# Performance work log

Hardware: AMD Instinct MI355X
Metric: run time of the kernel (lower is better)

## Reference

```python
import jax, jax.numpy as jnp
import numpy as np
from jax import lax

B, T, H, V, P, L = 256, 100, 1024, 47, 3, 3
BEGIN_IDX = 1  # SmilesCharDictionary.begin_idx


def setup_inputs() -> dict:
    key = jax.random.key(0)
    ks = jax.random.split(key, 10)
    s = 0.05
    return {
        "x": jax.random.randint(ks[0], (B, T), 0, V),
        "properties": jax.random.normal(ks[1], (B, P), dtype=jnp.float32),
        "h0": jnp.zeros((L, B, H), jnp.float32),
        "c0": jnp.zeros((L, B, H), jnp.float32),
        "E": jax.random.normal(ks[2], (V, H), dtype=jnp.float32) * s,
        "W_ih0": jax.random.normal(ks[3], (4 * H, H + P), dtype=jnp.float32) * s,
        "W_hh0": jax.random.normal(ks[4], (4 * H, H), dtype=jnp.float32) * s,
        "b_ih0": jnp.zeros((4 * H,), jnp.float32),
        "b_hh0": jnp.zeros((4 * H,), jnp.float32),
        "W_ih_r": jax.random.normal(ks[5], (L - 1, 4 * H, H), dtype=jnp.float32) * s,
        "W_hh_r": jax.random.normal(ks[6], (L - 1, 4 * H, H), dtype=jnp.float32) * s,
        "b_ih_r": jnp.zeros((L - 1, 4 * H), jnp.float32),
        "b_hh_r": jnp.zeros((L - 1, 4 * H), jnp.float32),
        "W_dec": jax.random.normal(ks[7], (V, H), dtype=jnp.float32) * s,
        "b_dec": jnp.zeros((V,), jnp.float32),
        "seq_len": T,
    }


def _lstm_cell(gates, c):
    # PyTorch gate order: i, f, g, o
    i, f, g, o = jnp.split(gates, 4, axis=-1)
    i = jax.nn.sigmoid(i)
    f = jax.nn.sigmoid(f)
    o = jax.nn.sigmoid(o)
    g = jnp.tanh(g)
    c_new = f * c + i * g
    return o * jnp.tanh(c_new), c_new


def _forward(x, properties, h0, c0, E, W_ih0, W_hh0, b_ih0, b_hh0,
             W_ih_r, W_hh_r, b_ih_r, b_hh_r, W_dec, b_dec, seq_len):
    b = properties.shape[0]
    steps = seq_len - 1  # loop runs t = 1 .. seq_len-1
    # Teacher-forcing inputs: [begin, x[:,1], ..., x[:,seq_len-2]] (x[:,0] is unused)
    begin = jnp.full((b, 1), BEGIN_IDX, dtype=x.dtype)
    tokens = jnp.concatenate([begin, x[:, 1:seq_len - 1]], axis=1)  # [B, steps]
    emb = E[tokens]  # [B, steps, H]
    props = jnp.broadcast_to(properties[:, None, :], (b, steps, properties.shape[1]))
    inp0 = jnp.concatenate([emb, props], axis=-1)  # [B, steps, H+P]
    # Precompute layer-0 input contribution to the gates (one big GEMM)
    gx0 = jnp.einsum('bti,gi->btg', inp0, W_ih0) + b_ih0  # [B, steps, 4H]

    n_layers = h0.shape[0]

    def step(carry, gx_t):
        h, c = carry  # each [L, B, H]
        gates = gx_t + h[0] @ W_hh0.T + b_hh0
        h_new, c_new = _lstm_cell(gates, c[0])
        hs, cs = [h_new], [c_new]
        xl = h_new
        for l in range(n_layers - 1):
            gates = xl @ W_ih_r[l].T + b_ih_r[l] + h[l + 1] @ W_hh_r[l].T + b_hh_r[l]
            h_new, c_new = _lstm_cell(gates, c[l + 1])
            hs.append(h_new)
            cs.append(c_new)
            xl = h_new
        return (jnp.stack(hs), jnp.stack(cs)), xl

    (hT, cT), outs = lax.scan(step, (h0, c0), gx0.transpose(1, 0, 2))
    outs = outs.transpose(1, 0, 2)  # [B, steps, H]
    logits = jnp.einsum('bth,vh->btv', outs, W_dec) + b_dec  # [B, steps, V]
    return logits, hT, cT


def reference(x, properties, h0, c0, E, W_ih0, W_hh0, b_ih0, b_hh0,
              W_ih_r, W_hh_r, b_ih_r, b_hh_r, W_dec, b_dec, seq_len):
    return _forward(x, properties, h0, c0, E, W_ih0, W_hh0, b_ih0, b_hh0,
                    W_ih_r, W_hh_r, b_ih_r, b_hh_r, W_dec, b_dec, seq_len)
```

## Files before the change

kernel.cpp:

```cpp
#include <hip/hip_runtime.h>


typedef unsigned short u16;
typedef __bf16 bf16x8 __attribute__((ext_vector_type(8)));
typedef float f32x4 __attribute__((ext_vector_type(4)));
typedef u16 u16x8 __attribute__((ext_vector_type(8)));

#define MFMA16(a,b,c) __builtin_amdgcn_mfma_f32_16x16x32_bf16((a),(b),(c),0,0,0)
#define BH 262144

__device__ __forceinline__ u16 f2bf(float f){
  unsigned u = __builtin_bit_cast(unsigned, f);
  u += 0x7fffu + ((u >> 16) & 1u);
  return (u16)(u >> 16);
}
__device__ __forceinline__ float bf2f(u16 s){
  unsigned u = ((unsigned)s) << 16;
  return __builtin_bit_cast(float, u);
}
__device__ __forceinline__ float sigm(float x){ return 1.f/(1.f+__expf(-x)); }
__device__ __forceinline__ float tanhfast(float x){ return 1.f - 2.f/(__expf(2.f*x)+1.f); }

__device__ __forceinline__ void ld_lds16(const u16* g, u16* l){
  __builtin_amdgcn_global_load_lds((const __attribute__((address_space(1))) void*)g,
                                   (__attribute__((address_space(3))) void*)l, 16, 0, 0);
}

__global__ void k_conv(const float* __restrict__ src, u16* __restrict__ dst,
                       long total, int srow, int sstride, int dstride, int doff){
  long i = ((long)blockIdx.x*blockDim.x + threadIdx.x)*8;
  if (i >= total) return;
  long r = i / srow;
  int  k = (int)(i - r*srow);
  const float* s = src + r*(long)sstride + k;
  u16x8 o;
  #pragma unroll
  for (int j=0;j<8;++j) o[j] = f2bf(s[j]);
  *(u16x8*)(dst + r*(long)dstride + doff + k) = o;
}

__global__ void k_repackB(const float* __restrict__ Wih, const float* __restrict__ Whh,
                          u16* __restrict__ dst, int nkt){
  long p = (long)blockIdx.x*256 + threadIdx.x;
  int G = (int)(p & 511);
  long q = p >> 9;
  int kt = (int)(q % nkt);
  int jt = (int)(q / nkt);
  int r = G >> 3, s = G & 7;
  int kk = kt*64 + ((s ^ (r & 7)) << 3);
  int n = (r >> 4)*1024 + jt*16 + (r & 15);
  const float* src = (kk < 1024) ? Wih + (size_t)n*1024 + kk
                                 : Whh + (size_t)n*1024 + (kk - 1024);
  u16x8 o;
  #pragma unroll
  for (int j=0;j<8;++j) o[j] = f2bf(src[j]);
  *(u16x8*)(dst + p*8) = o;
}

__global__ void k_misc(const float* __restrict__ b_ih0, const float* __restrict__ b_hh0,
                       const float* __restrict__ b_ihr, const float* __restrict__ b_hhr,
                       const float* __restrict__ h0, const float* __restrict__ c0,
                       const float* __restrict__ props, const float* __restrict__ W_ih0,
                       u16* __restrict__ Ebf, u16* __restrict__ Wdec,
                       float* __restrict__ bias0, float* __restrict__ bcat,
                       u16* __restrict__ hist0, u16* __restrict__ hist1,
                       u16* __restrict__ outsbF,
                       float* __restrict__ cst, float* __restrict__ gxp){
  long i = (long)blockIdx.x*256 + threadIdx.x;
  if (i < 4096){ bias0[i] = b_ih0[i] + b_hh0[i]; return; }
  i -= 4096;
  if (i < 2*4096){ bcat[i] = b_ihr[i] + b_hhr[i]; return; }
  i -= 2*4096;
  if (i < 1024){ Ebf[47*1024 + i] = 0; Wdec[47*1024 + i] = 0; return; }
  i -= 1024;
  if (i < (long)3*BH){
    int l = (int)(i >> 18); long r = i & (BH-1);
    u16 v = f2bf(h0[i]);
    if (l==0)      hist0[(size_t)7*BH + r] = v;
    else if (l==1) hist1[(size_t)7*BH + r] = v;
    else           outsbF[r] = v;
    cst[i] = c0[i];
    return;
  }
  i -= (long)3*BH;
  if (i < (long)256*4096){
    int b = (int)(i >> 12), n = (int)(i & 4095);
    const float* wr = W_ih0 + (long)n*1027 + 1024;
    gxp[i] = props[b*3+0]*wr[0] + props[b*3+1]*wr[1] + props[b*3+2]*wr[2];
  }
}

__global__ __launch_bounds__(64)
void k_gxemb(const u16* __restrict__ Ebf, const u16* __restrict__ Wih0b, float* __restrict__ gxe){
  const int lane = threadIdx.x;
  const int cl = lane & 15, ko = (lane >> 4)*8;
  const int m0 = blockIdx.x*16;
  const int n0 = blockIdx.y*16;
  f32x4 acc = {0.f,0.f,0.f,0.f};
  const u16* ap = Ebf   + (size_t)(m0+cl)*1024 + ko;
  const u16* bp = Wih0b + (size_t)(n0+cl)*1024 + ko;
  for (int k0=0; k0<1024; k0+=32){
    bf16x8 a = *(const bf16x8*)(ap + k0);
    bf16x8 b = *(const bf16x8*)(bp + k0);
    acc = MFMA16(a, b, acc);
  }
  const int rbase = (lane >> 4)*4;
  #pragma unroll
  for (int q=0;q<4;++q){
    int v = m0 + rbase + q;
    if (v < 47) gxe[(size_t)v*4096 + n0 + cl] = acc[q];
  }
}

#define KLOOP_BODY(APTR_EXPR)                                                   \
  auto stage = [&](int s, int kt){                                              \
    const int kbase = kt*64;                                                    \
    u16* sA = lds + (size_t)s*12288;                                            \
    u16* sB = sA + 8192;                                                        \
    _Pragma("unroll")                                                           \
    for (int j=0;j<4;++j){                                                      \
      int G = j*256 + tid; int r = G >> 3;                                      \
      int kk = kbase + (((G & 7) ^ (r & 7)) << 3);                              \
      ld_lds16(APTR_EXPR, sA + (size_t)G*8);                                    \
    }                                                                           \
    _Pragma("unroll")                                                           \
    for (int j=0;j<2;++j){                                                      \
      int G = j*256 + tid;                                                      \
      ld_lds16(Bblk + (size_t)kt*4096 + (size_t)G*8, sB + (size_t)G*8);         \
    }                                                                           \
  };                                                                            \
  f32x4 acc[2][4];                                                              \
  _Pragma("unroll")                                                             \
  for (int mf=0; mf<2; ++mf)                                                    \
    _Pragma("unroll")                                                           \
    for (int g=0; g<4; ++g) acc[mf][g] = (f32x4){0.f,0.f,0.f,0.f};              \
  stage(0,0); stage(1,1);                                                       \
  for (int kt=0; kt<16; ++kt){                                                  \
    if (kt == 15) asm volatile("s_waitcnt vmcnt(0)" ::: "memory");              \
    else          asm volatile("s_waitcnt vmcnt(6)" ::: "memory");              \
    __builtin_amdgcn_s_barrier();                                               \
    asm volatile("" ::: "memory");                                              \
    if (kt+2 < 16) stage((kt+2)%3, kt+2);                                       \
    const u16* A = lds + (size_t)(kt%3)*12288;                                  \
    const u16* B = A + 8192;                                                    \
    __builtin_amdgcn_s_setprio(1);                                              \
    _Pragma("unroll")                                                           \
    for (int half=0; half<2; ++half){                                           \
      const int kg = half*4 + hi;                                               \
      bf16x8 a0, a1, b[4];                                                      \
      { int r = m0w + cl;      a0 = *(const bf16x8*)(A + r*64 + ((kg ^ (r&7))<<3)); } \
      { int r = m0w + 16 + cl; a1 = *(const bf16x8*)(A + r*64 + ((kg ^ (r&7))<<3)); } \
      _Pragma("unroll")                                                         \
      for (int g=0; g<4; ++g){                                                  \
        int r = g*16 + cl;                                                      \
        b[g] = *(const bf16x8*)(B + r*64 + ((kg ^ (r&7))<<3));                  \
      }                                                                         \
      _Pragma("unroll")                                                         \
      for (int g=0; g<4; ++g){                                                  \
        acc[0][g] = MFMA16(a0, b[g], acc[0][g]);                                \
        acc[1][g] = MFMA16(a1, b[g], acc[1][g]);                                \
      }                                                                         \
    }                                                                           \
    __builtin_amdgcn_s_setprio(0);                                              \
    asm volatile("" ::: "memory");                                              \
  }

template<int LAYER>
__device__ __forceinline__ void diagh_tile(int mt, int jt, int t,
    const int* __restrict__ x, const u16* hp, u16* aux, float* cc,
    const u16* __restrict__ Bblk, const float* __restrict__ bias,
    const float* __restrict__ gxe, const float* __restrict__ gxp,
    const u16* xpt, u16* lds)
{
  const int tid = threadIdx.x;
  const int lane = tid & 63, w = tid >> 6;
  const int cl = lane & 15, hi = lane >> 4;
  const int m_base = mt*128, m0w = w*32;

  KLOOP_BODY(hp + (size_t)(m_base + r)*1024 + kk)

  const int hcol = jt*16 + cl;
  const float bi_ = bias[hcol], bf_ = bias[1024+hcol],
              bg_ = bias[2048+hcol], bo_ = bias[3072+hcol];
  #pragma unroll
  for (int mf=0; mf<2; ++mf){
    #pragma unroll
    for (int q=0; q<4; ++q){
      const int row = m_base + m0w + mf*16 + hi*4 + q;
      float gi = acc[mf][0][q] + bi_;
      float gf = acc[mf][1][q] + bf_;
      float gg = acc[mf][2][q] + bg_;
      float go = acc[mf][3][q] + bo_;
      if (LAYER == 0){
        const int tok = (t==0) ? 1 : x[row*100 + t];
        const float* ge = gxe + (size_t)tok*4096;
        const float* gp = gxp + (size_t)row*4096;
        gi += ge[hcol]        + gp[hcol];
        gf += ge[1024 + hcol] + gp[1024 + hcol];
        gg += ge[2048 + hcol] + gp[2048 + hcol];
        go += ge[3072 + hcol] + gp[3072 + hcol];
      } else {
        const u16* xr = xpt + (size_t)row*4096;
        gi += bf2f(xr[hcol]);
        gf += bf2f(xr[1024 + hcol]);
        gg += bf2f(xr[2048 + hcol]);
        go += bf2f(xr[3072 + hcol]);
      }
      const float i_ = sigm(gi), f_ = sigm(gf), o_ = sigm(go), g_ = tanhfast(gg);
      const size_t off = (size_t)row*1024 + hcol;
      const float cn = f_*cc[off] + i_*g_;
      cc[off] = cn;
      aux[off] = f2bf(o_*tanhfast(cn));
    }
  }
}

__device__ __forceinline__ void xp_tile(int m_base, int jt,
    const u16* hp, const u16* __restrict__ Bblk, u16* xpo, u16* lds)
{
  const int tid = threadIdx.x;
  const int lane = tid & 63, w = tid >> 6;
  const int cl = lane & 15, hi = lane >> 4;
  const int m0w = w*32;

  KLOOP_BODY(hp + (size_t)(m_base + r)*1024 + kk)

  const int hcol = jt*16 + cl;
  #pragma unroll
  for (int mf=0; mf<2; ++mf){
    #pragma unroll
    for (int q=0; q<4; ++q){
      const int m = m_base + m0w + mf*16 + hi*4 + q;
      u16* xr = xpo + (size_t)m*4096 + hcol;
      xr[0]    = f2bf(acc[mf][0][q]);
      xr[1024] = f2bf(acc[mf][1][q]);
      xr[2048] = f2bf(acc[mf][2][q]);
      xr[3072] = f2bf(acc[mf][3][q]);
    }
  }
}

__global__ __launch_bounds__(256)
void k_diag(int d, const int* __restrict__ x, u16* hist0, u16* hist1, u16* outsbF,
            float* __restrict__ cst, const u16* __restrict__ WpkH,
            const u16* __restrict__ WpkI,
            const float* __restrict__ bias0, const float* __restrict__ bcat,
            const float* __restrict__ gxe, const float* __restrict__ gxp,
            u16* __restrict__ xpb1, u16* __restrict__ xpb2)
{
  extern __shared__ u16 lds[];
  const int id = blockIdx.x;
  if (id < 384){
    const int mt = id / 192;
    const int slot = id - mt*192;
    const int layer = slot >> 6;
    const int jt = slot & 63;
    const int t = d - 3*layer;
    if (t < 0 || t > 98) return;
    if (layer == 0){
      diagh_tile<0>(mt, jt, t, x, hist0 + (size_t)((t+7)&7)*BH, hist0 + (size_t)(t&7)*BH,
                    cst, WpkH + (size_t)jt*65536, bias0, gxe, gxp, nullptr, lds);
    } else if (layer == 1){
      const u16* xpt = xpb1 + (size_t)((((t>>1)&1)<<1) + (t&1))*1048576;
      diagh_tile<1>(mt, jt, t, x, hist1 + (size_t)((t+7)&7)*BH, hist1 + (size_t)(t&7)*BH,
                    cst + BH, WpkH + (size_t)4194304 + (size_t)jt*65536, bcat,
                    nullptr, nullptr, xpt, lds);
    } else {
      const u16* xpt = xpb2 + (size_t)((((t>>1)&1)<<1) + (t&1))*1048576;
      diagh_tile<2>(mt, jt, t, x, outsbF + (size_t)t*BH, outsbF + (size_t)(t+1)*BH,
                    cst + 2*BH, WpkH + (size_t)8388608 + (size_t)jt*65536, bcat + 4096,
                    nullptr, nullptr, xpt, lds);
    }
  } else {
    const int idx = id - 384;
    const int mtx = idx >> 6, jt = idx & 63;
    const int tsub = mtx >> 1, m_base = (mtx & 1)*128;
    int w; const u16* hist; const u16* Wblk; u16* xpo;
    if ((d & 1) == 0){ w = (d-2)>>1; hist = hist0; Wblk = WpkI;                     xpo = xpb1; }
    else             { w = (d-5)>>1; hist = hist1; Wblk = WpkI + (size_t)4194304;   xpo = xpb2; }
    const int t = 2*w + tsub;
    if (t > 98) return;
    xp_tile(m_base, jt, hist + (size_t)(t&7)*BH, Wblk + (size_t)jt*65536,
            xpo + (size_t)(((w&1)<<1) + tsub)*1048576, lds);
  }
}

__global__ __launch_bounds__(256)
void k_decode(const u16* __restrict__ outs, const u16* __restrict__ Wdec,
              const float* __restrict__ bdec, float* __restrict__ logits){
  const int lane = threadIdx.x & 63, w = threadIdx.x >> 6;
  const int cl = lane & 15, ko = (lane >> 4)*8;
  const size_t m0 = ((size_t)blockIdx.x*4 + w)*16;
  const u16* ap = outs + (m0+cl)*1024 + ko;
  f32x4 acc[3];
  #pragma unroll
  for (int nt=0; nt<3; ++nt) acc[nt] = (f32x4){0.f,0.f,0.f,0.f};
  const u16* bp = Wdec + (size_t)cl*1024 + ko;
  for (int k0=0; k0<1024; k0+=32){
    bf16x8 a = *(const bf16x8*)(ap + k0);
    #pragma unroll
    for (int nt=0; nt<3; ++nt){
      bf16x8 b = *(const bf16x8*)(bp + (size_t)nt*16*1024 + k0);
      acc[nt] = MFMA16(a, b, acc[nt]);
    }
  }
  const int rbase = (lane >> 4)*4;
  #pragma unroll
  for (int nt=0; nt<3; ++nt){
    #pragma unroll
    for (int q=0; q<4; ++q){
      int v = nt*16 + cl;
      if (v < 47){
        size_t row = m0 + rbase + q;
        int tt = (int)(row >> 8);
        int b  = (int)(row & 255);
        logits[((size_t)b*99 + tt)*47 + v] = acc[nt][q] + bdec[v];
      }
    }
  }
}

__global__ void k_final(const u16* __restrict__ h0s, const u16* __restrict__ h1s,
                        const u16* __restrict__ h2s, const float* __restrict__ cst,
                        float* __restrict__ out){
  long i = (long)blockIdx.x*256 + threadIdx.x;
  if (i < (long)3*BH){
    int l = (int)(i >> 18); long r = i & (BH-1);
    const u16* src = (l==0) ? h0s : (l==1) ? h1s : h2s;
    out[1191168 + i] = bf2f(src[r]);
    out[1191168 + 786432 + i] = cst[i];
  }
}

extern "C" void kernel_launch(void* const* d_in, const int* in_sizes, int n_in,
                              void* d_out, int out_size, void* d_ws, size_t ws_size,
                              hipStream_t stream) {
  (void)in_sizes; (void)n_in; (void)out_size; (void)ws_size;
  const int*   x      = (const int*)  d_in[0];
  const float* props  = (const float*)d_in[1];
  const float* h0     = (const float*)d_in[2];
  const float* c0     = (const float*)d_in[3];
  const float* E      = (const float*)d_in[4];
  const float* W_ih0  = (const float*)d_in[5];
  const float* W_hh0  = (const float*)d_in[6];
  const float* b_ih0  = (const float*)d_in[7];
  const float* b_hh0  = (const float*)d_in[8];
  const float* W_ih_r = (const float*)d_in[9];
  const float* W_hh_r = (const float*)d_in[10];
  const float* b_ih_r = (const float*)d_in[11];
  const float* b_hh_r = (const float*)d_in[12];
  const float* W_dec  = (const float*)d_in[13];
  const float* b_dec  = (const float*)d_in[14];
  float* out = (float*)d_out;

  u16* WpkH   = (u16*)d_ws;
  u16* WpkI   = WpkH  + (size_t)12582912;
  u16* Wdec   = WpkI  + (size_t)8388608;
  u16* Ebf    = Wdec  + (size_t)49152;
  u16* hist0  = Ebf   + (size_t)49152;
  u16* hist1  = hist0 + (size_t)8*BH;
  u16* outsbF = hist1 + (size_t)8*BH;
  u16* xpb1   = outsbF + (size_t)100*BH;
  u16* xpb2   = xpb1  + (size_t)4194304;
  u16* Wih0b  = xpb1;
  float* gxe   = (float*)(xpb2 + (size_t)4194304);
  float* gxp   = gxe   + (size_t)196608;
  float* bias0 = gxp   + (size_t)1048576;
  float* bcat  = bias0 + 4096;
  float* cst   = bcat  + 8192;

  k_repackB<<<2048, 256, 0, stream>>>(W_hh0, W_hh0, WpkH, 16);
  k_repackB<<<2048, 256, 0, stream>>>(W_hh_r, W_hh_r, WpkH + (size_t)4194304, 16);
  k_repackB<<<2048, 256, 0, stream>>>(W_hh_r + (size_t)4194304, W_hh_r + (size_t)4194304,
                                      WpkH + (size_t)8388608, 16);
  k_repackB<<<2048, 256, 0, stream>>>(W_ih_r, W_ih_r, WpkI, 16);
  k_repackB<<<2048, 256, 0, stream>>>(W_ih_r + (size_t)4194304, W_ih_r + (size_t)4194304,
                                      WpkI + (size_t)4194304, 16);
  k_conv<<<2048, 256, 0, stream>>>(W_ih0, Wih0b, (long)4096*1024, 1024, 1027, 1024, 0);
  k_conv<<<24,   256, 0, stream>>>(E,     Ebf,   (long)47*1024,   1024, 1024, 1024, 0);
  k_conv<<<24,   256, 0, stream>>>(W_dec, Wdec,  (long)47*1024,   1024, 1024, 1024, 0);
  k_misc<<<7221, 256, 0, stream>>>(b_ih0, b_hh0, b_ih_r, b_hh_r, h0, c0, props, W_ih0,
                                   Ebf, Wdec, bias0, bcat, hist0, hist1, outsbF, cst, gxp);
  k_gxemb<<<dim3(3,256), 64, 0, stream>>>(Ebf, Wih0b, gxe);

  (void)hipFuncSetAttribute(reinterpret_cast<const void*>(k_diag),
                            hipFuncAttributeMaxDynamicSharedMemorySize, 73728);
  for (int d = 0; d <= 104; ++d){
    bool hx = ((d & 1) == 0) ? (d >= 2 && d <= 100) : (d >= 5 && d <= 103);
    k_diag<<<384 + (hx ? 256 : 0), 256, 73728, stream>>>(
        d, x, hist0, hist1, outsbF, cst, WpkH, WpkI,
        bias0, bcat, gxe, gxp, xpb1, xpb2);
  }

  k_decode<<<396, 256, 0, stream>>>(outsbF + (size_t)BH, Wdec, b_dec, out);
  k_final<<<3072, 256, 0, stream>>>(hist0 + (size_t)2*BH, hist1 + (size_t)2*BH,
                                    outsbF + (size_t)99*BH, cst, out);
}
```

Before: 2.475 ms.

## Batch input projections over four timesteps and prefetch weights to L2

Restructures the diagonal wavefront schedule so the inter-layer input projections are computed for four timesteps per batch instead of two. Layers are now skewed by five diagonals and the xp buffers are doubled to hold four slots. Extra global_load_lds prefetches of weight tiles into a throwaway LDS region warm the cache ahead of use, with vmcnt waits adjusted to match. The layer-0 input-gate tables are stored as bf16 to cut bandwidth. The trade-offs are more launches (109 vs 105), larger LDS and workspace use, and some precision loss in the layer-0 gate contributions.

```diff
diff --git a/kernel.cpp b/kernel.cpp
--- a/kernel.cpp
+++ b/kernel.cpp
@@ -65,7 +65,7 @@
                        float* __restrict__ bias0, float* __restrict__ bcat,
                        u16* __restrict__ hist0, u16* __restrict__ hist1,
                        u16* __restrict__ outsbF,
-                       float* __restrict__ cst, float* __restrict__ gxp){
+                       float* __restrict__ cst, u16* __restrict__ gxp){
   long i = (long)blockIdx.x*256 + threadIdx.x;
   if (i < 4096){ bias0[i] = b_ih0[i] + b_hh0[i]; return; }
   i -= 4096;
@@ -86,12 +86,12 @@
   if (i < (long)256*4096){
     int b = (int)(i >> 12), n = (int)(i & 4095);
     const float* wr = W_ih0 + (long)n*1027 + 1024;
-    gxp[i] = props[b*3+0]*wr[0] + props[b*3+1]*wr[1] + props[b*3+2]*wr[2];
+    gxp[i] = f2bf(props[b*3+0]*wr[0] + props[b*3+1]*wr[1] + props[b*3+2]*wr[2]);
   }
 }
 
 __global__ __launch_bounds__(64)
-void k_gxemb(const u16* __restrict__ Ebf, const u16* __restrict__ Wih0b, float* __restrict__ gxe){
+void k_gxemb(const u16* __restrict__ Ebf, const u16* __restrict__ Wih0b, u16* __restrict__ gxe){
   const int lane = threadIdx.x;
   const int cl = lane & 15, ko = (lane >> 4)*8;
   const int m0 = blockIdx.x*16;
@@ -108,11 +108,12 @@
   #pragma unroll
   for (int q=0;q<4;++q){
     int v = m0 + rbase + q;
-    if (v < 47) gxe[(size_t)v*4096 + n0 + cl] = acc[q];
+    if (v < 47) gxe[(size_t)v*4096 + n0 + cl] = f2bf(acc[q]);
   }
 }
 
 #define KLOOP_BODY(APTR_EXPR)                                                   \
+  u16* const trash = lds + 36864;                                               \
   auto stage = [&](int s, int kt){                                              \
     const int kbase = kt*64;                                                    \
     u16* sA = lds + (size_t)s*12288;                                            \
@@ -129,6 +130,13 @@
       ld_lds16(Bblk + (size_t)kt*4096 + (size_t)G*8, sB + (size_t)G*8);         \
     }                                                                           \
   };                                                                            \
+  auto pret = [&](int kt){                                                      \
+    _Pragma("unroll")                                                           \
+    for (int j=0;j<2;++j){                                                      \
+      int G = j*256 + tid;                                                      \
+      ld_lds16(Bblk + (size_t)kt*4096 + (size_t)G*8, trash);                    \
+    }                                                                           \
+  };                                                                            \
   f32x4 acc[2][4];                                                              \
   _Pragma("unroll")                                                             \
   for (int mf=0; mf<2; ++mf)                                                    \
@@ -136,11 +144,16 @@
     for (int g=0; g<4; ++g) acc[mf][g] = (f32x4){0.f,0.f,0.f,0.f};              \
   stage(0,0); stage(1,1);                                                       \
   for (int kt=0; kt<16; ++kt){                                                  \
-    if (kt == 15) asm volatile("s_waitcnt vmcnt(0)" ::: "memory");              \
-    else          asm volatile("s_waitcnt vmcnt(6)" ::: "memory");              \
+    if (kt == 0)       asm volatile("s_waitcnt vmcnt(6)"  ::: "memory");        \
+    else if (kt == 1)  asm volatile("s_waitcnt vmcnt(8)"  ::: "memory");        \
+    else if (kt <= 12) asm volatile("s_waitcnt vmcnt(10)" ::: "memory");        \
+    else if (kt == 13) asm volatile("s_waitcnt vmcnt(8)"  ::: "memory");        \
+    else if (kt == 14) asm volatile("s_waitcnt vmcnt(6)"  ::: "memory");        \
+    else               asm volatile("s_waitcnt vmcnt(0)"  ::: "memory");        \
     __builtin_amdgcn_s_barrier();                                               \
     asm volatile("" ::: "memory");                                              \
     if (kt+2 < 16) stage((kt+2)%3, kt+2);                                       \
+    if (kt+4 < 16) pret(kt+4);                                                  \
     const u16* A = lds + (size_t)(kt%3)*12288;                                  \
     const u16* B = A + 8192;                                                    \
     __builtin_amdgcn_s_setprio(1);                                              \
@@ -169,7 +182,7 @@
 __device__ __forceinline__ void diagh_tile(int mt, int jt, int t,
     const int* __restrict__ x, const u16* hp, u16* aux, float* cc,
     const u16* __restrict__ Bblk, const float* __restrict__ bias,
-    const float* __restrict__ gxe, const float* __restrict__ gxp,
+    const u16* __restrict__ gxe, const u16* __restrict__ gxp,
     const u16* xpt, u16* lds)
 {
   const int tid = threadIdx.x;
@@ -193,12 +206,12 @@
       float go = acc[mf][3][q] + bo_;
       if (LAYER == 0){
         const int tok = (t==0) ? 1 : x[row*100 + t];
-        const float* ge = gxe + (size_t)tok*4096;
-        const float* gp = gxp + (size_t)row*4096;
-        gi += ge[hcol]        + gp[hcol];
-        gf += ge[1024 + hcol] + gp[1024 + hcol];
-        gg += ge[2048 + hcol] + gp[2048 + hcol];
-        go += ge[3072 + hcol] + gp[3072 + hcol];
+        const u16* ge = gxe + (size_t)tok*4096;
+        const u16* gp = gxp + (size_t)row*4096;
+        gi += bf2f(ge[hcol])        + bf2f(gp[hcol]);
+        gf += bf2f(ge[1024 + hcol]) + bf2f(gp[1024 + hcol]);
+        gg += bf2f(ge[2048 + hcol]) + bf2f(gp[2048 + hcol]);
+        go += bf2f(ge[3072 + hcol]) + bf2f(gp[3072 + hcol]);
       } else {
         const u16* xr = xpt + (size_t)row*4096;
         gi += bf2f(xr[hcol]);
@@ -245,7 +258,7 @@
             float* __restrict__ cst, const u16* __restrict__ WpkH,
             const u16* __restrict__ WpkI,
             const float* __restrict__ bias0, const float* __restrict__ bcat,
-            const float* __restrict__ gxe, const float* __restrict__ gxp,
+            const u16* __restrict__ gxe, const u16* __restrict__ gxp,
             u16* __restrict__ xpb1, u16* __restrict__ xpb2)
 {
   extern __shared__ u16 lds[];
@@ -255,33 +268,35 @@
     const int slot = id - mt*192;
     const int layer = slot >> 6;
     const int jt = slot & 63;
-    const int t = d - 3*layer;
+    const int t = d - 5*layer;
     if (t < 0 || t > 98) return;
     if (layer == 0){
       diagh_tile<0>(mt, jt, t, x, hist0 + (size_t)((t+7)&7)*BH, hist0 + (size_t)(t&7)*BH,
                     cst, WpkH + (size_t)jt*65536, bias0, gxe, gxp, nullptr, lds);
     } else if (layer == 1){
-      const u16* xpt = xpb1 + (size_t)((((t>>1)&1)<<1) + (t&1))*1048576;
+      const u16* xpt = xpb1 + (size_t)((((t>>2)&1)<<2) + (t&3))*1048576;
       diagh_tile<1>(mt, jt, t, x, hist1 + (size_t)((t+7)&7)*BH, hist1 + (size_t)(t&7)*BH,
                     cst + BH, WpkH + (size_t)4194304 + (size_t)jt*65536, bcat,
                     nullptr, nullptr, xpt, lds);
     } else {
-      const u16* xpt = xpb2 + (size_t)((((t>>1)&1)<<1) + (t&1))*1048576;
+      const u16* xpt = xpb2 + (size_t)((((t>>2)&1)<<2) + (t&3))*1048576;
       diagh_tile<2>(mt, jt, t, x, outsbF + (size_t)t*BH, outsbF + (size_t)(t+1)*BH,
                     cst + 2*BH, WpkH + (size_t)8388608 + (size_t)jt*65536, bcat + 4096,
                     nullptr, nullptr, xpt, lds);
     }
   } else {
     const int idx = id - 384;
-    const int mtx = idx >> 6, jt = idx & 63;
-    const int tsub = mtx >> 1, m_base = (mtx & 1)*128;
+    const int jt = idx & 63;
+    const int mtx = (idx >> 6) & 1;
+    const int tsub = idx >> 7;
+    const int m_base = mtx*128;
     int w; const u16* hist; const u16* Wblk; u16* xpo;
-    if ((d & 1) == 0){ w = (d-2)>>1; hist = hist0; Wblk = WpkI;                     xpo = xpb1; }
-    else             { w = (d-5)>>1; hist = hist1; Wblk = WpkI + (size_t)4194304;   xpo = xpb2; }
-    const int t = 2*w + tsub;
+    if ((d & 3) == 0){ w = (d-4)>>2; hist = hist0; Wblk = WpkI;                   xpo = xpb1; }
+    else             { w = (d-9)>>2; hist = hist1; Wblk = WpkI + (size_t)4194304; xpo = xpb2; }
+    const int t = 4*w + tsub;
     if (t > 98) return;
     xp_tile(m_base, jt, hist + (size_t)(t&7)*BH, Wblk + (size_t)jt*65536,
-            xpo + (size_t)(((w&1)<<1) + tsub)*1048576, lds);
+            xpo + (size_t)(((w&1)<<2) + tsub)*1048576, lds);
   }
 }
 
@@ -361,11 +376,11 @@
   u16* hist1  = hist0 + (size_t)8*BH;
   u16* outsbF = hist1 + (size_t)8*BH;
   u16* xpb1   = outsbF + (size_t)100*BH;
-  u16* xpb2   = xpb1  + (size_t)4194304;
+  u16* xpb2   = xpb1  + (size_t)8388608;
   u16* Wih0b  = xpb1;
-  float* gxe   = (float*)(xpb2 + (size_t)4194304);
-  float* gxp   = gxe   + (size_t)196608;
-  float* bias0 = gxp   + (size_t)1048576;
+  u16* gxe    = xpb2  + (size_t)8388608;
+  u16* gxp    = gxe   + (size_t)196608;
+  float* bias0 = (float*)(gxp + (size_t)1048576);
   float* bcat  = bias0 + 4096;
   float* cst   = bcat  + 8192;
 
@@ -384,10 +399,11 @@
   k_gxemb<<<dim3(3,256), 64, 0, stream>>>(Ebf, Wih0b, gxe);
 
   (void)hipFuncSetAttribute(reinterpret_cast<const void*>(k_diag),
-                            hipFuncAttributeMaxDynamicSharedMemorySize, 73728);
-  for (int d = 0; d <= 104; ++d){
-    bool hx = ((d & 1) == 0) ? (d >= 2 && d <= 100) : (d >= 5 && d <= 103);
-    k_diag<<<384 + (hx ? 256 : 0), 256, 73728, stream>>>(
+                            hipFuncAttributeMaxDynamicSharedMemorySize, 75776);
+  for (int d = 0; d <= 108; ++d){
+    bool hx = ((d & 3) == 0) ? (d >= 4 && d <= 100)
+            : ((d & 3) == 1) ? (d >= 9 && d <= 105) : false;
+    k_diag<<<384 + (hx ? 512 : 0), 256, 75776, stream>>>(
         d, x, hist0, hist1, outsbF, cst, WpkH, WpkI,
         bias0, bcat, gxe, gxp, xpb1, xpb2);
   }
```

Measured after the change: 2.747 ms. +11.0%, slower.
